# Kernel optimization log

Measured on AMD Instinct MI355X. Metric: run time of the kernel, lower is better.

Reference implementation:

```python
import jax, jax.numpy as jnp
import numpy as np

D_MODEL = 1024
D_HEAD = 64
MAX_REL = 8
B, T = 4, 4096


def setup_inputs() -> dict:
    key = jax.random.key(0)
    k1, k2, k3, k4, k5 = jax.random.split(key, 5)
    return {
        "x": jax.random.normal(k1, (B, T, D_MODEL), dtype=jnp.float32),
        "W_q": jax.random.normal(k2, (D_HEAD, D_MODEL), dtype=jnp.float32) * (1.0 / np.sqrt(D_MODEL)),
        "W_k": jax.random.normal(k3, (D_HEAD, D_MODEL), dtype=jnp.float32) * (1.0 / np.sqrt(D_MODEL)),
        "W_v": jax.random.normal(k4, (D_HEAD, D_MODEL), dtype=jnp.float32) * (1.0 / np.sqrt(D_MODEL)),
        "rel_emb": jax.random.normal(k5, (2 * MAX_REL + 1, 1), dtype=jnp.float32),
    }


def reference(x, W_q, W_k, W_v, rel_emb):
    Bb, Tt, _ = x.shape
    scale = jnp.sqrt(jnp.asarray(W_q.shape[0], dtype=x.dtype))
    # projections (Linear: x @ W.T)
    q = jnp.einsum("btd,hd->bth", x, W_q)
    k = jnp.einsum("btd,hd->bth", x, W_k)
    v = jnp.einsum("btd,hd->bth", x, W_v)
    scores = jnp.einsum("bth,bsh->bts", q, k) / scale  # [B,T,T]
    # relative position bias: rel_emb[clip(j-i, -M, M) + M]
    i_idx = jnp.arange(Tt)[:, None]
    j_idx = jnp.arange(Tt)[None, :]
    rel = jnp.clip(j_idx - i_idx, -MAX_REL, MAX_REL) + MAX_REL  # [T,T] int
    rel_bias = rel_emb[rel, 0]  # [T,T]
    scores = scores + rel_bias[None, :, :]
    causal = j_idx <= i_idx  # [T,T] lower-triangular
    scores = jnp.where(causal[None, :, :], scores, -jnp.inf)
    attn = jax.nn.softmax(scores, axis=-1)
    return jnp.einsum("bts,bsh->bth", attn, v)
```

## Files before the change

kernel.cpp:

```cpp
#include <hip/hip_runtime.h>
#include <hip/hip_bf16.h>

#define BT 4
#define TT 4096
#define DM 1024
#define DH 64
#define NRE 17
#define LOG2E 1.4426950408889634f

using bf16 = __hip_bfloat16;
typedef __attribute__((ext_vector_type(8))) short short8;
typedef __attribute__((ext_vector_type(4))) short short4v;
typedef __attribute__((ext_vector_type(4))) float float4v;

#define BC8(x) __builtin_bit_cast(short8, x)

static __device__ __forceinline__ short8 load8(const bf16* p) {
    return *reinterpret_cast<const short8*>(p);
}
static __device__ __forceinline__ short bfbits(float x) {
    return (short)__bfloat16_as_ushort(__float2bfloat16(x));
}
static __device__ __forceinline__ short8 pack8(float4v a, float4v b) {
    short8 r;
    r[0] = bfbits(a[0]); r[1] = bfbits(a[1]); r[2] = bfbits(a[2]); r[3] = bfbits(a[3]);
    r[4] = bfbits(b[0]); r[5] = bfbits(b[1]); r[6] = bfbits(b[2]); r[7] = bfbits(b[3]);
    return r;
}
static __device__ __forceinline__ void gload_lds16(const void* g, void* l) {
    __builtin_amdgcn_global_load_lds(
        (const __attribute__((address_space(1))) void*)g,
        (__attribute__((address_space(3))) void*)l, 16, 0, 0);
}
static __device__ __forceinline__ unsigned lds_addr(const void* p) {
    return (unsigned)(size_t)(const __attribute__((address_space(3))) void*)p;
}

#define DSR(dst, addr, off) \
    asm volatile("ds_read_b128 %0, %1 offset:" off : "=v"(dst) : "v"(addr))


__global__ __launch_bounds__(256) void w_prep(
    const float* __restrict__ Wq, const float* __restrict__ Wk,
    const float* __restrict__ Wv, bf16* __restrict__ Wswz)
{
    const unsigned g = blockIdx.x * 256 + threadIdx.x;
    const unsigned c    = g / 768;
    const unsigned rem  = g - c * 768;
    const unsigned pair = rem >> 3;
    const unsigned slot = rem & 7;
    const unsigned l    = slot ^ (pair & 7);
    const unsigned row  = 2 * pair + (l >> 2);
    const unsigned k    = 32 * c + (l & 3) * 8;
    const float* src = (row < 64) ? &Wq[(size_t)row * DM + k]
                     : (row < 128) ? &Wk[(size_t)(row - 64) * DM + k]
                                   : &Wv[(size_t)(row - 128) * DM + k];
    float4v a = *reinterpret_cast<const float4v*>(src);
    float4v b = *reinterpret_cast<const float4v*>(src + 4);
    *reinterpret_cast<short8*>(&Wswz[(size_t)g * 8]) = pack8(a, b);
}

__global__ __launch_bounds__(256, 2) void qkv_gemm(
    const float* __restrict__ x, const bf16* __restrict__ Wswz,
    bf16* __restrict__ Qb, bf16* __restrict__ Kswz, bf16* __restrict__ Vswz)
{
    __shared__ __align__(16) float xs[2][2048];
    __shared__ __align__(16) short Wls[2][12288];

    const int w    = threadIdx.x >> 6;
    const int lane = threadIdx.x & 63;
    const int quad = lane >> 4;
    const int l16  = lane & 15;
    const int half = w & 1;
    const int colh = w >> 1;
    const int row0 = blockIdx.x * 32;

    float4v acc[6];
#pragma unroll
    for (int i = 0; i < 6; i++) acc[i] = (float4v)(0.f);

    auto stage = [&](int c, int p) {
#pragma unroll
        for (int j = 0; j < 2; j++) {
            const int call = 2 * w + j;
            const int row  = 4 * call + (lane >> 4);
            const int pu   = lane & 15;
            const int gu   = (pu & 8) | ((pu ^ row) & 7);
            gload_lds16(&x[(size_t)(row0 + row) * DM + c * 64 + gu * 4],
                        &xs[p][call * 256]);
        }
#pragma unroll
        for (int j = 0; j < 6; j++) {
            const int call = 6 * w + j;
            gload_lds16(&Wswz[(size_t)(2 * c) * 6144 + call * 512 + lane * 8],
                        &Wls[p][call * 512]);
        }
    };

    const unsigned xlds = lds_addr(&xs[0][0]);
    const unsigned wlds = lds_addr(&Wls[0][0]);
    const int R        = 16 * half + l16;
    const int lo3_0    = (2 * quad)     ^ (R & 7);
    const int lo3_1    = (2 * quad + 1) ^ (R & 7);
    const int pairBase = 48 * colh + (l16 >> 1);
    const int physW    = ((l16 & 1) * 4 + quad) ^ ((l16 >> 1) & 7);

    stage(0, 0);

    for (int c = 0; c < 16; c++) {
        const int p = c & 1;
        __syncthreads();
        if (c + 1 < 16) stage(c + 1, p ^ 1);

        const unsigned xb  = xlds + (unsigned)(p * 8192) + R * 64 * 4;
        const unsigned xa0 = xb + lo3_0 * 16;
        const unsigned xa1 = xb + lo3_1 * 16;
        const unsigned wa  = wlds + (unsigned)(p * 24576) + pairBase * 128 + physW * 16;

        float4v x00, x01, x10, x11;
        float4v w00, w01, w02, w03, w04, w05, w10, w11, w12, w13, w14, w15;
        DSR(x00, xa0, "0");   DSR(x10, xa0, "128");
        DSR(x01, xa1, "0");   DSR(x11, xa1, "128");
        DSR(w00, wa, "0");     DSR(w01, wa, "1024");  DSR(w02, wa, "2048");
        DSR(w03, wa, "3072");  DSR(w04, wa, "4096");  DSR(w05, wa, "5120");
        DSR(w10, wa, "12288"); DSR(w11, wa, "13312"); DSR(w12, wa, "14336");
        DSR(w13, wa, "15360"); DSR(w14, wa, "16384"); DSR(w15, wa, "17408");
        asm volatile("s_waitcnt lgkmcnt(0)"
            : "+v"(x00), "+v"(x01), "+v"(x10), "+v"(x11),
              "+v"(w00), "+v"(w01), "+v"(w02), "+v"(w03), "+v"(w04), "+v"(w05),
              "+v"(w10), "+v"(w11), "+v"(w12), "+v"(w13), "+v"(w14), "+v"(w15));

        short8 a0 = pack8(x00, x01);
        short8 a1 = pack8(x10, x11);
        acc[0] = __builtin_amdgcn_mfma_f32_16x16x32_bf16(a0, BC8(w00), acc[0], 0, 0, 0);
        acc[1] = __builtin_amdgcn_mfma_f32_16x16x32_bf16(a0, BC8(w01), acc[1], 0, 0, 0);
        acc[2] = __builtin_amdgcn_mfma_f32_16x16x32_bf16(a0, BC8(w02), acc[2], 0, 0, 0);
        acc[3] = __builtin_amdgcn_mfma_f32_16x16x32_bf16(a0, BC8(w03), acc[3], 0, 0, 0);
        acc[4] = __builtin_amdgcn_mfma_f32_16x16x32_bf16(a0, BC8(w04), acc[4], 0, 0, 0);
        acc[5] = __builtin_amdgcn_mfma_f32_16x16x32_bf16(a0, BC8(w05), acc[5], 0, 0, 0);
        acc[0] = __builtin_amdgcn_mfma_f32_16x16x32_bf16(a1, BC8(w10), acc[0], 0, 0, 0);
        acc[1] = __builtin_amdgcn_mfma_f32_16x16x32_bf16(a1, BC8(w11), acc[1], 0, 0, 0);
        acc[2] = __builtin_amdgcn_mfma_f32_16x16x32_bf16(a1, BC8(w12), acc[2], 0, 0, 0);
        acc[3] = __builtin_amdgcn_mfma_f32_16x16x32_bf16(a1, BC8(w13), acc[3], 0, 0, 0);
        acc[4] = __builtin_amdgcn_mfma_f32_16x16x32_bf16(a1, BC8(w14), acc[4], 0, 0, 0);
        acc[5] = __builtin_amdgcn_mfma_f32_16x16x32_bf16(a1, BC8(w15), acc[5], 0, 0, 0);
    }

    __syncthreads();
    short* Kimg = (short*)&xs[0][0];
    short* Vimg = Kimg + 2048;
#pragma unroll
    for (int nt = 0; nt < 6; nt++) {
        const int cc = 96 * colh + 16 * nt + l16;
#pragma unroll
        for (int r = 0; r < 4; r++) {
            const int jl = 16 * half + 4 * quad + r;
            const short hb = bfbits(acc[nt][r]);
            if (cc < 64) {
                Qb[(size_t)(row0 + jl) * DH + cc] = __hip_bfloat16_raw{(unsigned short)hb};
            } else if (cc < 128) {
                const int k  = cc - 64;
                const int h  = k >> 5;
                const int q2 = (k & 31) >> 3;
                Kimg[((2 * half + h) * 64 + q2 * 16 + 4 * quad + r) * 8 + (k & 7)] = hb;
            } else {
                const int d  = cc - 128;
                const int dh = d >> 5;
                const int hi = (d >> 4) & 1;
                Vimg[((2 * half + dh) * 64 + quad * 16 + (d & 15)) * 8 + hi * 4 + r] = hb;
            }
        }
    }
    __syncthreads();
    {
        const int b_     = row0 >> 12;
        const int tile32 = (row0 & (TT - 1)) >> 5;
        const size_t base = ((size_t)(b_ * 512 + tile32 * 4)) * 512;
        const int u = threadIdx.x;
        *reinterpret_cast<short8*>(&Kswz[base + (size_t)u * 8]) =
            *reinterpret_cast<const short8*>(&Kimg[u * 8]);
        *reinterpret_cast<short8*>(&Vswz[base + (size_t)u * 8]) =
            *reinterpret_cast<const short8*>(&Vimg[u * 8]);
    }
}

__global__ __launch_bounds__(512, 2) void attn(
    const bf16* __restrict__ Qb, const bf16* __restrict__ Kswz,
    const bf16* __restrict__ Vswz, const float* __restrict__ rel,
    float* __restrict__ out, float* __restrict__ part1, float* __restrict__ msl)
{
    __shared__ __align__(16) short sbuf[32768];

    const int w     = threadIdx.x >> 6;
    const int lane  = threadIdx.x & 63;
    const int quad  = lane >> 4;
    const int l16   = lane & 15;
    const int batch = blockIdx.x & 3;
    const int rest  = blockIdx.x >> 2;
    const int pr    = rest >> 1;
    const int hh    = rest & 1;
    const int s     = w + 8 * hh;

    const float SCL = 0.125f * LOG2E;
    float relreg = 0.f;
    if (lane < NRE) relreg = rel[lane] * LOG2E;
    const float rel0 = __shfl(relreg, 0, 64);

    const size_t bbase = (size_t)batch * TT;

    short* mybuf = &sbuf[w * 4096];
    const unsigned sbase = lds_addr(&sbuf[0]) + (unsigned)(w * 8192 + lane * 16);

    float* Osh = (float*)&sbuf[0];
    float* mM  = Osh + 4 * 32 * 68;
    float* lL  = mM + 256;

    auto stageKV = [&](int T) {
        const size_t gb = ((size_t)(batch * 512 + T * 4)) * 512;
#pragma unroll
        for (int j = 0; j < 4; j++)
            gload_lds16(&Kswz[gb + j * 512 + lane * 8], mybuf + j * 512);
#pragma unroll
        for (int j = 0; j < 4; j++)
            gload_lds16(&Vswz[gb + j * 512 + lane * 8], mybuf + 2048 + j * 512);
    };

#pragma unroll 1
    for (int ph = 0; ph < 2; ph++) {
        const int t  = ph ? (127 - pr) : pr;
        const int q0 = 32 * t;

        short8 bq[2][2];
#pragma unroll
        for (int qh = 0; qh < 2; qh++) {
            const bf16* qp = &Qb[(bbase + q0 + 16 * qh + l16) * DH];
            bq[qh][0] = load8(qp + quad * 8);
            bq[qh][1] = load8(qp + 32 + quad * 8);
        }
        __builtin_amdgcn_s_waitcnt(0xF70);

        float4v o[2][4];
#pragma unroll
        for (int qh = 0; qh < 2; qh++)
#pragma unroll
            for (int dt = 0; dt < 4; dt++) o[qh][dt] = (float4v)(0.f);
        float m_st[2] = {-1e30f, -1e30f}, l_st[2] = {0.f, 0.f};

        const int cnt = (t >= s) ? (((t - s) >> 4) + 1) : 0;
        if (cnt > 0) stageKV(s);

        for (int k = 0; k < cnt; k++) {
            const int T = s + 16 * k;
            __builtin_amdgcn_s_waitcnt(0xF70);

            float4v kf0, kf1, kf2, kf3, vf0, vf1, vf2, vf3;
            DSR(kf0, sbase, "0");    DSR(kf1, sbase, "1024");
            DSR(kf2, sbase, "2048"); DSR(kf3, sbase, "3072");
            DSR(vf0, sbase, "4096"); DSR(vf1, sbase, "5120");
            DSR(vf2, sbase, "6144"); DSR(vf3, sbase, "7168");
            asm volatile("s_waitcnt lgkmcnt(0)"
                : "+v"(kf0), "+v"(kf1), "+v"(kf2), "+v"(kf3),
                  "+v"(vf0), "+v"(vf1), "+v"(vf2), "+v"(vf3));

            if (k + 1 < cnt) stageKV(s + 16 * (k + 1));

            const int js = 32 * T;
#pragma unroll
            for (int qh = 0; qh < 2; qh++) {
                float4v st[2];
                st[0] = (float4v)(0.f); st[1] = (float4v)(0.f);
                __builtin_amdgcn_s_setprio(1);
                st[0] = __builtin_amdgcn_mfma_f32_16x16x32_bf16(BC8(kf0), bq[qh][0], st[0], 0, 0, 0);
                st[0] = __builtin_amdgcn_mfma_f32_16x16x32_bf16(BC8(kf1), bq[qh][1], st[0], 0, 0, 0);
                st[1] = __builtin_amdgcn_mfma_f32_16x16x32_bf16(BC8(kf2), bq[qh][0], st[1], 0, 0, 0);
                st[1] = __builtin_amdgcn_mfma_f32_16x16x32_bf16(BC8(kf3), bq[qh][1], st[1], 0, 0, 0);
                __builtin_amdgcn_s_setprio(0);

                const int i_row = q0 + 16 * qh + l16;
                float mcur = -1e30f;
                if (js + 40 <= q0 + 16 * qh) {
#pragma unroll
                    for (int n = 0; n < 2; n++)
#pragma unroll
                        for (int r = 0; r < 4; r++) {
                            float v = st[n][r] * SCL + rel0;
                            st[n][r] = v;
                            mcur = fmaxf(mcur, v);
                        }
                } else {
#pragma unroll
                    for (int n = 0; n < 2; n++) {
                        const int jb = js + 16 * n + 4 * quad;
#pragma unroll
                        for (int r = 0; r < 4; r++) {
                            const int d = jb + r - i_row;
                            int idx = d + 8;
                            idx = idx < 0 ? 0 : (idx > 16 ? 16 : idx);
                            float v = st[n][r] * SCL + __shfl(relreg, idx, 64);
                            v = (d > 0) ? -1e30f : v;
                            st[n][r] = v;
                            mcur = fmaxf(mcur, v);
                        }
                    }
                }

                mcur = fmaxf(mcur, __shfl_xor(mcur, 16, 64));
                mcur = fmaxf(mcur, __shfl_xor(mcur, 32, 64));

                if (__any(mcur > m_st[qh] + 8.f)) {
                    const float mn = fmaxf(m_st[qh], mcur);
                    const float alpha = exp2f(m_st[qh] - mn);
                    m_st[qh] = mn;
                    l_st[qh] *= alpha;
#pragma unroll
                    for (int dt = 0; dt < 4; dt++)
#pragma unroll
                        for (int r = 0; r < 4; r++) o[qh][dt][r] *= alpha;
                }
                const float mn = m_st[qh];

                float lsum = 0.f;
                short4v pb[2];
#pragma unroll
                for (int n = 0; n < 2; n++)
#pragma unroll
                    for (int r = 0; r < 4; r++) {
                        const float e = exp2f(st[n][r] - mn);
                        lsum += e;
                        pb[n][r] = bfbits(e);
                    }
                lsum += __shfl_xor(lsum, 16, 64);
                lsum += __shfl_xor(lsum, 32, 64);
                l_st[qh] += lsum;

                __builtin_amdgcn_s_setprio(1);
#pragma unroll
                for (int n = 0; n < 2; n++) {
#pragma unroll
                    for (int dh = 0; dh < 2; dh++) {
                        const short8 vs = BC8((dh == 0) ? ((n == 0) ? vf0 : vf2)
                                                        : ((n == 0) ? vf1 : vf3));
                        short4v lo, hi;
                        lo[0] = vs[0]; lo[1] = vs[1]; lo[2] = vs[2]; lo[3] = vs[3];
                        hi[0] = vs[4]; hi[1] = vs[5]; hi[2] = vs[6]; hi[3] = vs[7];
                        o[qh][2 * dh]     = __builtin_amdgcn_mfma_f32_16x16x16bf16_1k(lo, pb[n], o[qh][2 * dh], 0, 0, 0);
                        o[qh][2 * dh + 1] = __builtin_amdgcn_mfma_f32_16x16x16bf16_1k(hi, pb[n], o[qh][2 * dh + 1], 0, 0, 0);
                    }
                }
                __builtin_amdgcn_s_setprio(0);
            }
        }

        __syncthreads();
        if (w >= 4) {
            const int slot = w - 4;
#pragma unroll
            for (int qh = 0; qh < 2; qh++) {
                const int row = 16 * qh + l16;
                if (quad == 0) { mM[w * 32 + row] = m_st[qh]; lL[w * 32 + row] = l_st[qh]; }
#pragma unroll
                for (int dt = 0; dt < 4; dt++)
                    *reinterpret_cast<float4v*>(&Osh[(slot * 32 + row) * 68 + 16 * dt + 4 * quad]) = o[qh][dt];
            }
        }
        __syncthreads();
        if (w < 4) {
#pragma unroll
            for (int qh = 0; qh < 2; qh++) {
                const int row = 16 * qh + l16;
                const float mp = mM[(w + 4) * 32 + row], lp = lL[(w + 4) * 32 + row];
                const float M  = fmaxf(m_st[qh], mp);
                const float ea = exp2f(m_st[qh] - M);
                const float eb = exp2f(mp - M);
                const float ln = l_st[qh] * ea + lp * eb;
#pragma unroll
                for (int dt = 0; dt < 4; dt++) {
                    float4v op = *reinterpret_cast<float4v*>(&Osh[(w * 32 + row) * 68 + 16 * dt + 4 * quad]);
#pragma unroll
                    for (int r = 0; r < 4; r++) o[qh][dt][r] = o[qh][dt][r] * ea + op[r] * eb;
                }
                if (quad == 0) { mM[w * 32 + row] = M; lL[w * 32 + row] = ln; }
#pragma unroll
                for (int dt = 0; dt < 4; dt++)
                    *reinterpret_cast<float4v*>(&Osh[(w * 32 + row) * 68 + 16 * dt + 4 * quad]) = o[qh][dt];
            }
        }
        __syncthreads();
        {
            const int q = batch * 128 + t;
            float* ob = hh ? (part1 + (size_t)q * 2048)
                           : (out + ((size_t)bbase + q0) * DH);
            float* ml = msl + (size_t)(q * 2 + hh) * 64;
            for (int idx = threadIdx.x; idx < 32 * 64; idx += 512) {
                const int row = idx >> 6;
                const int col = idx & 63;
                float M = mM[row];
#pragma unroll
                for (int s2 = 1; s2 < 4; s2++) M = fmaxf(M, mM[s2 * 32 + row]);
                float L = 0.f, a = 0.f;
#pragma unroll
                for (int s2 = 0; s2 < 4; s2++) {
                    const float ex = exp2f(mM[s2 * 32 + row] - M);
                    L += lL[s2 * 32 + row] * ex;
                    a += Osh[(s2 * 32 + row) * 68 + col] * ex;
                }
                ob[idx] = a;
                if (col == 0) { ml[row] = M; ml[32 + row] = L; }
            }
        }
        __syncthreads();
    }
}

__global__ __launch_bounds__(256) void attn_merge(
    const float* __restrict__ part1, const float* __restrict__ msl,
    float* __restrict__ out)
{
    const int q = blockIdx.x;
    const int batch = q >> 7, t = q & 127;
    float* ob0 = out + ((size_t)batch * TT + t * 32) * DH;
    const float* o1  = part1 + (size_t)q * 2048;
    const float* ml0 = msl + (size_t)(q * 2 + 0) * 64;
    const float* ml1 = msl + (size_t)(q * 2 + 1) * 64;
    for (int idx = threadIdx.x; idx < 32 * 64; idx += 256) {
        const int row = idx >> 6;
        const float m0 = ml0[row], m1 = ml1[row];
        const float l0 = ml0[32 + row], l1 = ml1[32 + row];
        const float M  = fmaxf(m0, m1);
        const float e0 = exp2f(m0 - M), e1 = exp2f(m1 - M);
        const float den = l0 * e0 + l1 * e1;
        const float num = ob0[idx] * e0 + o1[idx] * e1;
        ob0[idx] = num / den;
    }
}

extern "C" void kernel_launch(void* const* d_in, const int* in_sizes, int n_in,
                              void* d_out, int out_size, void* d_ws, size_t ws_size,
                              hipStream_t stream)
{
    const float* x   = (const float*)d_in[0];
    const float* Wq  = (const float*)d_in[1];
    const float* Wk  = (const float*)d_in[2];
    const float* Wv  = (const float*)d_in[3];
    const float* rel = (const float*)d_in[4];
    float* out = (float*)d_out;

    bf16* Qb   = (bf16*)d_ws;
    bf16* Kswz = Qb   + (size_t)BT * TT * DH;
    bf16* Vswz = Kswz + (size_t)BT * TT * DH;
    bf16* Wswz = Vswz + (size_t)BT * TT * DH;
    float* part1 = (float*)(Wswz + 24576 * 8);
    float* msl   = part1 + (size_t)512 * 2048;

    w_prep<<<96, 256, 0, stream>>>(Wq, Wk, Wv, Wswz);
    qkv_gemm<<<512, 256, 0, stream>>>(x, Wswz, Qb, Kswz, Vswz);
    attn<<<512, 512, 0, stream>>>(Qb, Kswz, Vswz, rel, out, part1, msl);
    attn_merge<<<512, 256, 0, stream>>>(part1, msl, out);
}
```

Baseline: 163.1 us.

## Load K/V fragments directly from global into registers, drop LDS staging

Replaces the per-wave global-to-LDS async staging and LDS reads of K/V tiles with direct global loads into registers, prefetching the next tile after the current tile's last use. This removes the LDS round-trip and waitcnt barriers and shrinks shared memory to only the reduction buffers, which may allow higher occupancy. In exchange, global load latency is less hidden because each prefetch is issued late in the iteration and consumed at the start of the next one.

New measurement: 156.1 us. 1.04x faster.

```diff
diff --git a/kernel.cpp b/kernel.cpp
--- a/kernel.cpp
+++ b/kernel.cpp
@@ -189,7 +189,7 @@
     const bf16* __restrict__ Vswz, const float* __restrict__ rel,
     float* __restrict__ out, float* __restrict__ part1, float* __restrict__ msl)
 {
-    __shared__ __align__(16) short sbuf[32768];
+    __shared__ __align__(16) float smem[9216];
 
     const int w     = threadIdx.x >> 6;
     const int lane  = threadIdx.x & 63;
@@ -208,22 +208,11 @@
 
     const size_t bbase = (size_t)batch * TT;
 
-    short* mybuf = &sbuf[w * 4096];
-    const unsigned sbase = lds_addr(&sbuf[0]) + (unsigned)(w * 8192 + lane * 16);
-
-    float* Osh = (float*)&sbuf[0];
+    float* Osh = smem;
     float* mM  = Osh + 4 * 32 * 68;
     float* lL  = mM + 256;
 
-    auto stageKV = [&](int T) {
-        const size_t gb = ((size_t)(batch * 512 + T * 4)) * 512;
-#pragma unroll
-        for (int j = 0; j < 4; j++)
-            gload_lds16(&Kswz[gb + j * 512 + lane * 8], mybuf + j * 512);
-#pragma unroll
-        for (int j = 0; j < 4; j++)
-            gload_lds16(&Vswz[gb + j * 512 + lane * 8], mybuf + 2048 + j * 512);
-    };
+    const unsigned loff = (unsigned)lane * 8;
 
 #pragma unroll 1
     for (int ph = 0; ph < 2; ph++) {
@@ -237,7 +226,6 @@
             bq[qh][0] = load8(qp + quad * 8);
             bq[qh][1] = load8(qp + 32 + quad * 8);
         }
-        __builtin_amdgcn_s_waitcnt(0xF70);
 
         float4v o[2][4];
 #pragma unroll
@@ -247,34 +235,36 @@
         float m_st[2] = {-1e30f, -1e30f}, l_st[2] = {0.f, 0.f};
 
         const int cnt = (t >= s) ? (((t - s) >> 4) + 1) : 0;
-        if (cnt > 0) stageKV(s);
+
+        short8 K0, K1, K2, K3, V0, V1, V2, V3;
+        if (cnt > 0) {
+            const bf16* kp = Kswz + ((size_t)(batch * 512 + s * 4)) * 512 + loff;
+            const bf16* vp = Vswz + ((size_t)(batch * 512 + s * 4)) * 512 + loff;
+            K0 = load8(kp);        K1 = load8(kp + 512);
+            K2 = load8(kp + 1024); K3 = load8(kp + 1536);
+            V0 = load8(vp);        V1 = load8(vp + 512);
+            V2 = load8(vp + 1024); V3 = load8(vp + 1536);
+        }
 
         for (int k = 0; k < cnt; k++) {
-            const int T = s + 16 * k;
-            __builtin_amdgcn_s_waitcnt(0xF70);
-
-            float4v kf0, kf1, kf2, kf3, vf0, vf1, vf2, vf3;
-            DSR(kf0, sbase, "0");    DSR(kf1, sbase, "1024");
-            DSR(kf2, sbase, "2048"); DSR(kf3, sbase, "3072");
-            DSR(vf0, sbase, "4096"); DSR(vf1, sbase, "5120");
-            DSR(vf2, sbase, "6144"); DSR(vf3, sbase, "7168");
-            asm volatile("s_waitcnt lgkmcnt(0)"
-                : "+v"(kf0), "+v"(kf1), "+v"(kf2), "+v"(kf3),
-                  "+v"(vf0), "+v"(vf1), "+v"(vf2), "+v"(vf3));
-
-            if (k + 1 < cnt) stageKV(s + 16 * (k + 1));
-
+            const int T  = s + 16 * k;
             const int js = 32 * T;
 #pragma unroll
             for (int qh = 0; qh < 2; qh++) {
                 float4v st[2];
                 st[0] = (float4v)(0.f); st[1] = (float4v)(0.f);
                 __builtin_amdgcn_s_setprio(1);
-                st[0] = __builtin_amdgcn_mfma_f32_16x16x32_bf16(BC8(kf0), bq[qh][0], st[0], 0, 0, 0);
-                st[0] = __builtin_amdgcn_mfma_f32_16x16x32_bf16(BC8(kf1), bq[qh][1], st[0], 0, 0, 0);
-                st[1] = __builtin_amdgcn_mfma_f32_16x16x32_bf16(BC8(kf2), bq[qh][0], st[1], 0, 0, 0);
-                st[1] = __builtin_amdgcn_mfma_f32_16x16x32_bf16(BC8(kf3), bq[qh][1], st[1], 0, 0, 0);
+                st[0] = __builtin_amdgcn_mfma_f32_16x16x32_bf16(K0, bq[qh][0], st[0], 0, 0, 0);
+                st[0] = __builtin_amdgcn_mfma_f32_16x16x32_bf16(K1, bq[qh][1], st[0], 0, 0, 0);
+                st[1] = __builtin_amdgcn_mfma_f32_16x16x32_bf16(K2, bq[qh][0], st[1], 0, 0, 0);
+                st[1] = __builtin_amdgcn_mfma_f32_16x16x32_bf16(K3, bq[qh][1], st[1], 0, 0, 0);
                 __builtin_amdgcn_s_setprio(0);
+
+                if (qh == 1 && k + 1 < cnt) {
+                    const bf16* kp = Kswz + ((size_t)(batch * 512 + (T + 16) * 4)) * 512 + loff;
+                    K0 = load8(kp);        K1 = load8(kp + 512);
+                    K2 = load8(kp + 1024); K3 = load8(kp + 1536);
+                }
 
                 const int i_row = q0 + 16 * qh + l16;
                 float mcur = -1e30f;
@@ -338,8 +328,8 @@
                 for (int n = 0; n < 2; n++) {
 #pragma unroll
                     for (int dh = 0; dh < 2; dh++) {
-                        const short8 vs = BC8((dh == 0) ? ((n == 0) ? vf0 : vf2)
-                                                        : ((n == 0) ? vf1 : vf3));
+                        const short8 vs = (dh == 0) ? ((n == 0) ? V0 : V2)
+                                                    : ((n == 0) ? V1 : V3);
                         short4v lo, hi;
                         lo[0] = vs[0]; lo[1] = vs[1]; lo[2] = vs[2]; lo[3] = vs[3];
                         hi[0] = vs[4]; hi[1] = vs[5]; hi[2] = vs[6]; hi[3] = vs[7];
@@ -348,6 +338,12 @@
                     }
                 }
                 __builtin_amdgcn_s_setprio(0);
+
+                if (qh == 1 && k + 1 < cnt) {
+                    const bf16* vp = Vswz + ((size_t)(batch * 512 + (T + 16) * 4)) * 512 + loff;
+                    V0 = load8(vp);        V1 = load8(vp + 512);
+                    V2 = load8(vp + 1024); V3 = load8(vp + 1536);
+                }
             }
         }
 
```
